# Performance work log

Measured on AMD Instinct MI355X. Metric: run time of the kernel, lower is better.

Reference implementation:

```python
import jax, jax.numpy as jnp
import numpy as np

D_MODEL = 1024
H = 16
D_K = D_MODEL // H
D_FF = 4096
EPS = 1e-6
NEG = -1.0e9


def setup_inputs() -> dict:
    key = jax.random.key(0)
    ks = jax.random.split(key, 8)
    B, S = 4, 2048
    x = jax.random.normal(ks[0], (B, S, D_MODEL), dtype=jnp.float32)
    src_mask = jnp.ones((B, 1, S, S), dtype=jnp.int32)
    s = 0.02
    wq = jax.random.normal(ks[1], (D_MODEL, D_MODEL), jnp.float32) * s
    wk = jax.random.normal(ks[2], (D_MODEL, D_MODEL), jnp.float32) * s
    wv = jax.random.normal(ks[3], (D_MODEL, D_MODEL), jnp.float32) * s
    wo = jax.random.normal(ks[4], (D_MODEL, D_MODEL), jnp.float32) * s
    w1 = jax.random.normal(ks[5], (D_MODEL, D_FF), jnp.float32) * s
    b1 = jnp.zeros((D_FF,), jnp.float32)
    w2 = jax.random.normal(ks[6], (D_FF, D_MODEL), jnp.float32) * s
    b2 = jnp.zeros((D_MODEL,), jnp.float32)
    # LayerNorm params are scalars in the original (torch.ones(1)/zeros(1))
    a1 = jnp.ones((1,), jnp.float32); bt1 = jnp.zeros((1,), jnp.float32)
    a2 = jnp.ones((1,), jnp.float32); bt2 = jnp.zeros((1,), jnp.float32)
    return {"x": x, "src_mask": src_mask, "wq": wq, "wk": wk, "wv": wv,
            "wo": wo, "w1": w1, "b1": b1, "w2": w2, "b2": b2,
            "a1": a1, "bt1": bt1, "a2": a2, "bt2": bt2}


def _layernorm(x, alpha, beta):
    # Original: (x - mean) / (std + eps), std with Bessel correction (torch default)
    mean = jnp.mean(x, axis=-1, keepdims=True)
    std = jnp.std(x, axis=-1, keepdims=True, ddof=1)
    return alpha * (x - mean) / (std + EPS) + beta


def _mha(x, mask, wq, wk, wv, wo):
    B, S, _ = x.shape
    q = (x @ wq).reshape(B, S, H, D_K).transpose(0, 2, 1, 3)  # [B,H,S,Dk]
    k = (x @ wk).reshape(B, S, H, D_K).transpose(0, 2, 1, 3)
    v = (x @ wv).reshape(B, S, H, D_K).transpose(0, 2, 1, 3)
    scores = jnp.einsum('bhqd,bhkd->bhqk', q, k) / jnp.sqrt(jnp.float32(D_K))
    scores = jnp.where(mask == 0, NEG, scores)
    attn = jax.nn.softmax(scores, axis=-1)
    out = jnp.einsum('bhqk,bhkd->bhqd', attn, v)  # [B,H,S,Dk]
    out = out.transpose(0, 2, 1, 3).reshape(B, S, D_MODEL)
    return out @ wo


def reference(x, src_mask, wq, wk, wv, wo, w1, b1, w2, b2, a1, bt1, a2, bt2):
    # Sublayer 1: self-attention with post-norm residual (dropout = eval/identity)
    attn_out = _mha(x, src_mask, wq, wk, wv, wo)
    x = _layernorm(x + attn_out, a1, bt1)
    # Sublayer 2: FFN with post-norm residual
    ffn_out = jax.nn.relu(x @ w1 + b1) @ w2 + b2
    x = _layernorm(x + ffn_out, a2, bt2)
    return x
```

## Files before the change

### kernel.cpp

```cpp
#include <hip/hip_runtime.h>
#include <stdint.h>

typedef __bf16 bf16x8 __attribute__((ext_vector_type(8)));
typedef float f32x4 __attribute__((ext_vector_type(4)));
typedef float f32x16 __attribute__((ext_vector_type(16)));
typedef unsigned short u16;
typedef u16 u16x8 __attribute__((ext_vector_type(8)));
typedef u16 u16x4 __attribute__((ext_vector_type(4)));
typedef uint32_t u32;

#define DEV __device__ __forceinline__
#define MFMA(a, b, c) __builtin_amdgcn_mfma_f32_16x16x32_bf16(a, b, c, 0, 0, 0)
#define MFMA32(a, b, c) __builtin_amdgcn_mfma_f32_32x32x16_bf16(a, b, c, 0, 0, 0)

static constexpr int B_ = 4, S_ = 2048, M_ = 8192, D_ = 1024, H_ = 16, DFF_ = 4096;

DEV u16 f2bf(float f) {
    union { float f; u32 u; } c; c.f = f;
    u32 u = c.u;
    return (u16)((u + 0x7fffu + ((u >> 16) & 1u)) >> 16);
}

DEV u32 cvt_pk_bf16(float lo, float hi) {
    u32 r;
    asm("v_cvt_pk_bf16_f32 %0, %1, %2" : "=v"(r) : "v"(lo), "v"(hi));
    return r;
}

DEV float v_exp2(float x) {
    float r;
    asm("v_exp_f32 %0, %1" : "=v"(r) : "v"(x));
    return r;
}

DEV void gload16(void* lds, const void* g) {
    __builtin_amdgcn_global_load_lds(
        (const __attribute__((address_space(1))) unsigned int*)g,
        (__attribute__((address_space(3))) unsigned int*)lds, 16, 0, 0);
}


__global__ __launch_bounds__(256) void k_pack_mask(const int* __restrict__ m,
                                                   u32* __restrict__ bits, int nwords) {
    int w = blockIdx.x * 256 + threadIdx.x;
    if (w >= nwords) return;
    const int4* s = (const int4*)(m + (size_t)w * 32);
    u32 r = 0;
#pragma unroll
    for (int j = 0; j < 8; j++) {
        int4 v = s[j];
        r |= (u32)(v.x != 0) << (j * 4) | (u32)(v.y != 0) << (j * 4 + 1) |
             (u32)(v.z != 0) << (j * 4 + 2) | (u32)(v.w != 0) << (j * 4 + 3);
    }
    bits[w] = r;
}

__global__ __launch_bounds__(256) void k_cast_bf16(const float* __restrict__ s,
                                                   u16* __restrict__ d, int n4) {
    int i = blockIdx.x * 256 + threadIdx.x;
    if (i >= n4) return;
    f32x4 v = ((const f32x4*)s)[i];
    u16x4 o;
    o[0] = f2bf(v[0]); o[1] = f2bf(v[1]); o[2] = f2bf(v[2]); o[3] = f2bf(v[3]);
    ((u16x4*)d)[i] = o;
}

__global__ void k_transpose_cast(const float* __restrict__ s, u16* __restrict__ d,
                                 int K, int N) {
    __shared__ float t[32][33];
    int n0 = blockIdx.x * 32, k0 = blockIdx.y * 32;
    int tx = threadIdx.x, ty = threadIdx.y;
#pragma unroll
    for (int i = 0; i < 4; i++)
        t[ty + i * 8][tx] = s[(size_t)(k0 + ty + i * 8) * N + n0 + tx];
    __syncthreads();
#pragma unroll
    for (int i = 0; i < 4; i++)
        d[(size_t)(n0 + ty + i * 8) * K + k0 + tx] = f2bf(t[tx][ty + i * 8]);
}

template <int EPI>
__global__ __launch_bounds__(512, 4) void k_gemm8(const u16* __restrict__ A,
                                                  const u16* __restrict__ Bt,
                                                  float* __restrict__ Cf,
                                                  u16* __restrict__ Cb,
                                                  const float* __restrict__ bias,
                                                  const float* __restrict__ resid,
                                                  u16* __restrict__ Vt,
                                                  int N, int K) {
    __shared__ u16 As[2][128 * 64];
    __shared__ u16 Bs[2][128 * 64];
    const int tid = threadIdx.x, lane = tid & 63, wave = tid >> 6;
    const int lr = lane & 15, lg = lane >> 4;
    const int wm = wave >> 1, wn = wave & 1;
    const int nbx = N >> 7;
    const int chunk = gridDim.x >> 3;
    const int id = ((int)blockIdx.x & 7) * chunk + ((int)blockIdx.x >> 3);
    const size_t row0 = (size_t)(id / nbx) * 128;
    const int col0 = (id % nbx) * 128;
    const int srow = lane >> 3;
    const int sgr = (lane & 7) ^ srow;
    const int NT = K >> 6;
    f32x4 acc[2][4] = {};

    auto stage = [&](int buf, int t) {
#pragma unroll
        for (int i = 0; i < 2; i++) {
            int c = i * 8 + wave;
            gload16((char*)&As[buf][0] + c * 1024,
                    (const char*)(A + (row0 + c * 8 + srow) * K + t * 64 + sgr * 8));
        }
#pragma unroll
        for (int i = 0; i < 2; i++) {
            int c = i * 8 + wave;
            gload16((char*)&Bs[buf][0] + c * 1024,
                    (const char*)(Bt + (size_t)(col0 + c * 8 + srow) * K + t * 64 + sgr * 8));
        }
    };

    stage(0, 0);
    for (int t = 0; t < NT; ++t) {
        const int cur = t & 1;
        if (t + 1 < NT) {
            stage(cur ^ 1, t + 1);
            asm volatile("s_waitcnt vmcnt(4)" ::: "memory");
        } else {
            asm volatile("s_waitcnt vmcnt(0)" ::: "memory");
        }
        __builtin_amdgcn_s_barrier();
        asm volatile("" ::: "memory");
        bf16x8 bF[4][2];
#pragma unroll
        for (int n = 0; n < 4; n++) {
            int r = wn * 64 + n * 16 + lr;
            int rb = r * 128, sw = (r & 7) << 4;
#pragma unroll
            for (int ks = 0; ks < 2; ks++)
                bF[n][ks] = *(const bf16x8*)((char*)&Bs[cur][0] +
                                             (rb + ((ks * 64 + lg * 16) ^ sw)));
        }
#pragma unroll
        for (int m = 0; m < 2; m++) {
            int r = wm * 32 + m * 16 + lr;
            int rb = r * 128, sw = (r & 7) << 4;
            bf16x8 a0 = *(const bf16x8*)((char*)&As[cur][0] + (rb + ((lg * 16) ^ sw)));
            bf16x8 a1 = *(const bf16x8*)((char*)&As[cur][0] + (rb + ((64 + lg * 16) ^ sw)));
            __builtin_amdgcn_s_setprio(1);
#pragma unroll
            for (int n = 0; n < 4; n++) {
                acc[m][n] = MFMA(a0, bF[n][0], acc[m][n]);
                acc[m][n] = MFMA(a1, bF[n][1], acc[m][n]);
            }
            __builtin_amdgcn_s_setprio(0);
        }
        asm volatile("" ::: "memory");
        __builtin_amdgcn_s_barrier();
    }
#pragma unroll
    for (int m = 0; m < 2; m++)
#pragma unroll
        for (int n = 0; n < 4; n++) {
            const int cg = col0 + wn * 64 + n * 16 + lr;
            const int rbase = (int)row0 + wm * 32 + m * 16 + lg * 4;
            if constexpr (EPI == 0) {
                const int proj = cg >> 10, hh = (cg >> 6) & 15, dk = cg & 63;
                const int b = rbase >> 11, s = rbase & 2047;
                if (proj == 2) {
                    u16x4 ov;
#pragma unroll
                    for (int i = 0; i < 4; i++) ov[i] = f2bf(acc[m][n][i]);
                    *(u16x4*)(Vt + ((size_t)(b * 16 + hh) * 64 + dk) * 2048 + s) = ov;
                } else {
                    const float sc = (proj == 0) ? 0.1803368801111832f : 1.f;
                    size_t base = ((size_t)(proj * 64 + b * 16 + hh) * 2048 + s) * 64 + dk;
#pragma unroll
                    for (int i = 0; i < 4; i++)
                        Cb[base + (size_t)i * 64] = f2bf(acc[m][n][i] * sc);
                }
            } else {
#pragma unroll
                for (int i = 0; i < 4; i++) {
                    const int rg = rbase + i;
                    float v = acc[m][n][i];
                    if constexpr (EPI == 1) {
                        Cf[(size_t)rg * N + cg] = v + resid[(size_t)rg * N + cg];
                    } else if constexpr (EPI == 2) {
                        v += bias[cg];
                        v = v > 0.f ? v : 0.f;
                        Cb[(size_t)rg * N + cg] = f2bf(v);
                    } else {
                        Cf[(size_t)rg * N + cg] = v + bias[cg] + resid[(size_t)rg * N + cg];
                    }
                }
            }
        }
}

template <int EPI>
__global__ __launch_bounds__(512, 2) void k_gemm256(const u16* __restrict__ A,
                                                    const u16* __restrict__ Bt,
                                                    float* __restrict__ Cf,
                                                    u16* __restrict__ Cb,
                                                    const float* __restrict__ bias,
                                                    int N, int K) {
    __shared__ u16 As[2][256 * 64];
    __shared__ u16 Bs[2][256 * 64];
    const int tid = threadIdx.x, lane = tid & 63, wave = tid >> 6;
    const int lr = lane & 15, lg = lane >> 4;
    const int wm = wave >> 2, wn = wave & 3;
    const int nbx = N >> 8;
    const int chunk = gridDim.x >> 3;
    const int id = ((int)blockIdx.x & 7) * chunk + ((int)blockIdx.x >> 3);
    const size_t row0 = (size_t)(id / nbx) * 256;
    const int col0 = (id % nbx) * 256;
    const int srow = lane >> 3;
    const int sgr = (lane & 7) ^ srow;
    const int NT = K >> 6;
    f32x4 acc[8][4] = {};

    auto stage_half = [&](int isB, int buf, int t, int h) {
        const u16* g = isB ? Bt : A;
        const size_t grow0 = isB ? (size_t)col0 : row0;
        char* base = isB ? (char*)&Bs[buf][0] : (char*)&As[buf][0];
#pragma unroll
        for (int l = 0; l < 2; l++) {
            int rt = h * 128 + l * 64 + wave * 8;
            gload16(base + rt * 128,
                    (const char*)(g + (grow0 + rt + srow) * K + t * 64 + sgr * 8));
        }
    };
    auto rdA = [&](int cur, int mh, int m, int kk) -> bf16x8 {
        int r = wm * 128 + mh * 64 + m * 16 + lr;
        int gi = kk * 4 + lg;
        return *(const bf16x8*)((char*)&As[cur][0] + r * 128 + ((gi ^ (r & 7)) << 4));
    };
    auto rdB = [&](int cur, int nh, int n, int kk) -> bf16x8 {
        int r = wn * 64 + nh * 32 + n * 16 + lr;
        int gi = kk * 4 + lg;
        return *(const bf16x8*)((char*)&Bs[cur][0] + r * 128 + ((gi ^ (r & 7)) << 4));
    };

    stage_half(0, 0, 0, 0); stage_half(0, 0, 0, 1);
    stage_half(1, 0, 0, 0); stage_half(1, 0, 0, 1);
    stage_half(1, 1, 1, 0); stage_half(1, 1, 1, 1);
    asm volatile("s_waitcnt vmcnt(4)" ::: "memory");
    __builtin_amdgcn_s_barrier();

    bf16x8 aF[4][2], b0F[2][2], b1F[2][2];
    for (int t = 0; t < NT; ++t) {
        const int cur = t & 1, nxt = cur ^ 1;
#pragma unroll
        for (int m = 0; m < 4; m++) { aF[m][0] = rdA(cur, 0, m, 0); aF[m][1] = rdA(cur, 0, m, 1); }
#pragma unroll
        for (int n = 0; n < 2; n++) { b0F[n][0] = rdB(cur, 0, n, 0); b0F[n][1] = rdB(cur, 0, n, 1); }
        if (t + 1 < NT) stage_half(0, nxt, t + 1, 0);
        __builtin_amdgcn_s_barrier();
        asm volatile("s_waitcnt lgkmcnt(0)" ::: "memory");
        __builtin_amdgcn_sched_barrier(0);
        __builtin_amdgcn_s_setprio(1);
#pragma unroll
        for (int m = 0; m < 4; m++)
#pragma unroll
            for (int n = 0; n < 2; n++) {
                acc[m][n] = MFMA(aF[m][0], b0F[n][0], acc[m][n]);
                acc[m][n] = MFMA(aF[m][1], b0F[n][1], acc[m][n]);
            }
        __builtin_amdgcn_s_setprio(0);
        __builtin_amdgcn_s_barrier();
#pragma unroll
        for (int n = 0; n < 2; n++) { b1F[n][0] = rdB(cur, 1, n, 0); b1F[n][1] = rdB(cur, 1, n, 1); }
        if (t + 1 < NT) stage_half(0, nxt, t + 1, 1);
        __builtin_amdgcn_s_barrier();
        asm volatile("s_waitcnt lgkmcnt(0)" ::: "memory");
        __builtin_amdgcn_sched_barrier(0);
        __builtin_amdgcn_s_setprio(1);
#pragma unroll
        for (int m = 0; m < 4; m++)
#pragma unroll
            for (int n = 0; n < 2; n++) {
                acc[m][2 + n] = MFMA(aF[m][0], b1F[n][0], acc[m][2 + n]);
                acc[m][2 + n] = MFMA(aF[m][1], b1F[n][1], acc[m][2 + n]);
            }
        __builtin_amdgcn_s_setprio(0);
        __builtin_amdgcn_s_barrier();
#pragma unroll
        for (int m = 0; m < 4; m++) { aF[m][0] = rdA(cur, 1, m, 0); aF[m][1] = rdA(cur, 1, m, 1); }
        if (t + 2 < NT) stage_half(1, cur, t + 2, 0);
        __builtin_amdgcn_s_barrier();
        asm volatile("s_waitcnt lgkmcnt(0)" ::: "memory");
        __builtin_amdgcn_sched_barrier(0);
        __builtin_amdgcn_s_setprio(1);
#pragma unroll
        for (int m = 0; m < 4; m++)
#pragma unroll
            for (int n = 0; n < 2; n++) {
                acc[4 + m][2 + n] = MFMA(aF[m][0], b1F[n][0], acc[4 + m][2 + n]);
                acc[4 + m][2 + n] = MFMA(aF[m][1], b1F[n][1], acc[4 + m][2 + n]);
            }
        __builtin_amdgcn_s_setprio(0);
        __builtin_amdgcn_s_barrier();
        if (t + 2 < NT) stage_half(1, cur, t + 2, 1);
        if (t + 1 < NT) {
            if (t + 2 < NT) asm volatile("s_waitcnt vmcnt(4)" ::: "memory");
            else            asm volatile("s_waitcnt vmcnt(0)" ::: "memory");
        }
        __builtin_amdgcn_s_barrier();
        __builtin_amdgcn_s_setprio(1);
#pragma unroll
        for (int m = 0; m < 4; m++)
#pragma unroll
            for (int n = 0; n < 2; n++) {
                acc[4 + m][n] = MFMA(aF[m][0], b0F[n][0], acc[4 + m][n]);
                acc[4 + m][n] = MFMA(aF[m][1], b0F[n][1], acc[4 + m][n]);
            }
        __builtin_amdgcn_s_setprio(0);
        __builtin_amdgcn_s_barrier();
    }
#pragma unroll
    for (int m = 0; m < 8; m++)
#pragma unroll
        for (int n = 0; n < 4; n++)
#pragma unroll
            for (int i = 0; i < 4; i++) {
                int rg = (int)row0 + wm * 128 + m * 16 + lg * 4 + i;
                int cg = col0 + wn * 64 + n * 16 + lr;
                float v = acc[m][n][i];
                if constexpr (EPI == 2) {
                    v += bias[cg];
                    v = v > 0.f ? v : 0.f;
                    Cb[(size_t)rg * N + cg] = f2bf(v);
                } else {
                    Cf[(size_t)rg * N + cg] = v;
                }
            }
}

__global__ __launch_bounds__(256) void k_attn(const u16* __restrict__ qkv,
                                              const u16* __restrict__ vT,
                                              const u32* __restrict__ mbits,
                                              u16* __restrict__ outb) {
    __shared__ u16 Kt[2][64 * 64];
    __shared__ u16 Vt[2][64 * 64];
    __shared__ u32 pm[2][128][2];
    const int tid = threadIdx.x, lane = tid & 63, wave = tid >> 6;
    const int l31 = lane & 31, hi = lane >> 5;
    const int id0 = blockIdx.y * 16 + blockIdx.x;
    const int id = (id0 & 7) * 128 + (id0 >> 3);
    const int bh = id >> 4;
    const int b = bh >> 4, h = bh & 15;
    const int qb0 = (id & 15) * 128;
    const size_t qbase = (size_t)bh * (2048 * 64);
    const size_t kbase = (size_t)(64 + bh) * (2048 * 64);
    const size_t vtbase = (size_t)bh * (64 * 2048);

    bf16x8 qf[4];
    const int q0 = qb0 + wave * 32;
#pragma unroll
    for (int dstep = 0; dstep < 4; dstep++)
        qf[dstep] = *(const bf16x8*)(qkv + qbase + (size_t)(q0 + l31) * 64 +
                                     dstep * 16 + hi * 8);

    u16x8 ones_u;
#pragma unroll
    for (int e = 0; e < 8; e++) ones_u[e] = 0x3f80;
    const bf16x8 ones8 = *(const bf16x8*)&ones_u;

    f32x16 o0 = {}, o1 = {}, lacc = {};
    f32x16 zin;
#pragma unroll
    for (int r = 0; r < 16; r++) zin[r] = -16.f;

    const int str = tid >> 2, sq = tid & 3;
    const int swzs = (str & 7) << 4;

    u16x8 krA, krB, vrA, vrB; u32 mwA;
    auto issue_loads = [&](int kv0n) {
        const u16* ksrc = qkv + kbase + (size_t)(kv0n + str) * 64 + sq * 16;
        krA = *(const u16x8*)ksrc; krB = *(const u16x8*)(ksrc + 8);
        const u16* vsrc = vT + vtbase + (size_t)str * 2048 + kv0n + sq * 16;
        vrA = *(const u16x8*)vsrc; vrB = *(const u16x8*)(vsrc + 8);
        mwA = mbits[(size_t)(b * 2048 + qb0 + (tid >> 1)) * 64 + (kv0n >> 5) + (tid & 1)];
    };
    auto write_tile = [&](int buf) -> bool {
        int b0 = str * 128 + sq * 32;
        *(u16x8*)((char*)&Kt[buf][0] + ((b0) ^ swzs)) = krA;
        *(u16x8*)((char*)&Kt[buf][0] + ((b0 + 16) ^ swzs)) = krB;
        *(u16x8*)((char*)&Vt[buf][0] + ((b0) ^ swzs)) = vrA;
        *(u16x8*)((char*)&Vt[buf][0] + ((b0 + 16) ^ swzs)) = vrB;
        pm[buf][tid >> 1][tid & 1] = mwA;
        return (__ballot(mwA == 0xffffffffu) == ~0ull);
    };

    const int rK0 = l31, rK1 = 32 + l31;
    const int swK0 = (rK0 & 7) << 4, swK1 = (rK1 & 7) << 4;

    issue_loads(0);
    bool aon_nxt = write_tile(0);
    for (int t = 0; t < 32; ++t) {
        const int cur = t & 1;
        const bool aon_cur = aon_nxt;
        if (t + 1 < 32) issue_loads((t + 1) * 64);
        asm volatile("s_waitcnt lgkmcnt(0)" ::: "memory");
        __builtin_amdgcn_s_barrier();

        f32x16 st0 = zin, st1 = zin;
        __builtin_amdgcn_s_setprio(1);
#pragma unroll
        for (int dstep = 0; dstep < 4; dstep++) {
            bf16x8 kf0 = *(const bf16x8*)((char*)&Kt[cur][0] + rK0 * 128 +
                                          ((dstep * 32 + hi * 16) ^ swK0));
            bf16x8 kf1 = *(const bf16x8*)((char*)&Kt[cur][0] + rK1 * 128 +
                                          ((dstep * 32 + hi * 16) ^ swK1));
            st0 = MFMA32(kf0, qf[dstep], st0);
            st1 = MFMA32(kf1, qf[dstep], st1);
        }
        __builtin_amdgcn_s_setprio(0);

        if (!aon_cur) {
            u32 mw0 = pm[cur][wave * 32 + l31][0] >> (hi * 4);
            u32 mw1 = pm[cur][wave * 32 + l31][1] >> (hi * 4);
#pragma unroll
            for (int r = 0; r < 16; r++) {
                int sh = (r & 3) + 8 * (r >> 2);
                if (!((mw0 >> sh) & 1u)) st0[r] = -1e9f;
                if (!((mw1 >> sh) & 1u)) st1[r] = -1e9f;
            }
        }
        bf16x8 pa[4];
#pragma unroll
        for (int r = 0; r < 16; r++) { st0[r] = v_exp2(st0[r]); st1[r] = v_exp2(st1[r]); }
#pragma unroll
        for (int kvb = 0; kvb < 2; kvb++) {
            const f32x16& st = kvb ? st1 : st0;
            u32 wA[4], wB[4];
#pragma unroll
            for (int g = 0; g < 4; g++) {
                wA[g] = cvt_pk_bf16(st[4 * g], st[4 * g + 1]);
                wB[g] = cvt_pk_bf16(st[4 * g + 2], st[4 * g + 3]);
            }
#pragma unroll
            for (int s = 0; s < 2; s++) {
                u32 xA = wA[2 * s], yA = wA[2 * s + 1];
                asm("v_permlane32_swap_b32 %0, %1" : "+v"(xA), "+v"(yA));
                u32 xB = wB[2 * s], yB = wB[2 * s + 1];
                asm("v_permlane32_swap_b32 %0, %1" : "+v"(xB), "+v"(yB));
                union { u32 w[4]; bf16x8 v; } pk;
                pk.w[0] = xA; pk.w[1] = xB; pk.w[2] = yA; pk.w[3] = yB;
                pa[kvb * 2 + s] = pk.v;
            }
        }
        __builtin_amdgcn_s_setprio(1);
#pragma unroll
        for (int ks = 0; ks < 4; ks++) {
            bf16x8 vb0 = *(const bf16x8*)((char*)&Vt[cur][0] + rK0 * 128 +
                                          ((ks * 32 + hi * 16) ^ swK0));
            bf16x8 vb1 = *(const bf16x8*)((char*)&Vt[cur][0] + rK1 * 128 +
                                          ((ks * 32 + hi * 16) ^ swK1));
            lacc = MFMA32(pa[ks], ones8, lacc);
            o0 = MFMA32(pa[ks], vb0, o0);
            o1 = MFMA32(pa[ks], vb1, o1);
        }
        __builtin_amdgcn_s_setprio(0);
        if (t + 1 < 32) aon_nxt = write_tile(cur ^ 1);
    }
#pragma unroll
    for (int r = 0; r < 16; r++) {
        float inv = 1.f / lacc[r];
        int qg = qb0 + wave * 32 + (r & 3) + 8 * (r >> 2) + 4 * hi;
        size_t rowb = (size_t)(b * 2048 + qg) * 1024 + h * 64 + l31;
        outb[rowb] = f2bf(o0[r] * inv);
        outb[rowb + 32] = f2bf(o1[r] * inv);
    }
}

template <bool WB>
__global__ __launch_bounds__(256) void k_ln(const float* __restrict__ tin,
                                            float* __restrict__ outf,
                                            u16* __restrict__ outb,
                                            const float* __restrict__ alpha,
                                            const float* __restrict__ beta) {
    const int row = blockIdx.x, tid = threadIdx.x;
    const f32x4 t = ((const f32x4*)(tin + (size_t)row * 1024))[tid];
    float s = t[0] + t[1] + t[2] + t[3];
    float ss = t[0] * t[0] + t[1] * t[1] + t[2] * t[2] + t[3] * t[3];
#pragma unroll
    for (int m2 = 1; m2 < 64; m2 <<= 1) {
        s += __shfl_xor(s, m2);
        ss += __shfl_xor(ss, m2);
    }
    __shared__ float ps[4], pss[4];
    if ((tid & 63) == 0) { ps[tid >> 6] = s; pss[tid >> 6] = ss; }
    __syncthreads();
    s = ps[0] + ps[1] + ps[2] + ps[3];
    ss = pss[0] + pss[1] + pss[2] + pss[3];
    const float mean = s * (1.f / 1024.f);
    float var = (ss - 1024.f * mean * mean) * (1.f / 1023.f);
    var = fmaxf(var, 0.f);
    const float inv = alpha[0] / (sqrtf(var) + 1e-6f);
    const float bet = beta[0];
    f32x4 oo;
#pragma unroll
    for (int i = 0; i < 4; i++) oo[i] = (t[i] - mean) * inv + bet;
    ((f32x4*)(outf + (size_t)row * 1024))[tid] = oo;
    if constexpr (WB) {
        u16x4 ob;
#pragma unroll
        for (int i = 0; i < 4; i++) ob[i] = f2bf(oo[i]);
        ((u16x4*)(outb + (size_t)row * 1024))[tid] = ob;
    }
}

extern "C" void kernel_launch(void* const* d_in, const int* in_sizes, int n_in,
                              void* d_out, int out_size, void* d_ws, size_t ws_size,
                              hipStream_t stream) {
    const float* x   = (const float*)d_in[0];
    const int*   msk = (const int*)d_in[1];
    const float* wq  = (const float*)d_in[2];
    const float* wk  = (const float*)d_in[3];
    const float* wv  = (const float*)d_in[4];
    const float* wo  = (const float*)d_in[5];
    const float* w1  = (const float*)d_in[6];
    const float* b1  = (const float*)d_in[7];
    const float* w2  = (const float*)d_in[8];
    const float* b2  = (const float*)d_in[9];
    const float* a1  = (const float*)d_in[10];
    const float* bt1 = (const float*)d_in[11];
    const float* a2  = (const float*)d_in[12];
    const float* bt2 = (const float*)d_in[13];
    float* out = (float*)d_out;

    char* ws = (char*)d_ws;
    size_t off = 0;
    auto alloc = [&](size_t bytes) {
        void* p = ws + off;
        off += (bytes + 255) & ~(size_t)255;
        return p;
    };
    u16* xb    = (u16*)alloc((size_t)M_ * D_ * 2);
    u16* wqkvT = (u16*)alloc((size_t)3 * D_ * D_ * 2);
    u16* woT   = (u16*)alloc((size_t)D_ * D_ * 2);
    u16* w1T   = (u16*)alloc((size_t)DFF_ * D_ * 2);
    u16* w2T   = (u16*)alloc((size_t)D_ * DFF_ * 2);
    u32* mbits = (u32*)alloc((size_t)B_ * S_ * 64 * 4);
    u16* aout  = (u16*)alloc((size_t)M_ * D_ * 2);
    float* y   = (float*)alloc((size_t)M_ * D_ * 4);
    float* x1  = (float*)alloc((size_t)M_ * D_ * 4);
    u16* x1b   = (u16*)alloc((size_t)M_ * D_ * 2);
    u16* vTb   = (u16*)alloc((size_t)64 * 64 * 2048 * 2);
    u16* qkv   = (u16*)alloc((size_t)M_ * DFF_ * 2);
    u16* hft   = qkv;

    k_pack_mask<<<dim3((B_ * S_ * 64) / 256), 256, 0, stream>>>(msk, mbits, B_ * S_ * 64);
    k_cast_bf16<<<dim3((M_ * D_ / 4) / 256), 256, 0, stream>>>(x, xb, M_ * D_ / 4);
    dim3 tb(32, 8);
    k_transpose_cast<<<dim3(32, 32), tb, 0, stream>>>(wq, wqkvT, D_, D_);
    k_transpose_cast<<<dim3(32, 32), tb, 0, stream>>>(wk, wqkvT + D_ * D_, D_, D_);
    k_transpose_cast<<<dim3(32, 32), tb, 0, stream>>>(wv, wqkvT + 2 * D_ * D_, D_, D_);
    k_transpose_cast<<<dim3(32, 32), tb, 0, stream>>>(wo, woT, D_, D_);
    k_transpose_cast<<<dim3(128, 32), tb, 0, stream>>>(w1, w1T, D_, DFF_);
    k_transpose_cast<<<dim3(32, 128), tb, 0, stream>>>(w2, w2T, DFF_, D_);

    k_gemm8<0><<<dim3(1536), 512, 0, stream>>>(xb, wqkvT, nullptr, qkv, nullptr,
                                               nullptr, vTb, 3 * D_, D_);
    k_attn<<<dim3(16, 64), 256, 0, stream>>>(qkv, vTb, mbits, aout);
    k_gemm8<1><<<dim3(512), 512, 0, stream>>>(aout, woT, y, nullptr, nullptr, x,
                                              nullptr, D_, D_);
    k_ln<true><<<dim3(M_), 256, 0, stream>>>(y, x1, x1b, a1, bt1);
    k_gemm256<2><<<dim3(512), 512, 0, stream>>>(x1b, w1T, nullptr, hft, b1, DFF_, D_);
    k_gemm8<3><<<dim3(512), 512, 0, stream>>>(hft, w2T, y, nullptr, b2, x1,
                                              nullptr, D_, DFF_);
    k_ln<false><<<dim3(M_), 256, 0, stream>>>(y, out, nullptr, a2, bt2);
}
```

Measured before the change: 412.4 us.

## Use split-K 256-tile GEMM for FFN down-projection and fuse partial sums into LayerNorm

The second FFN GEMM (K=4096) moves from the 128-tile kernel to the 256x256 tile kernel with a two-way split over K. Each half writes its own fp32 partial output, and a new LayerNorm kernel adds the two partials, the residual and the bias before normalising. The four square weight transpose-casts are also merged into one launch using a z grid dimension. The larger tiles raise data reuse, but the grid is only 256 blocks, and the extra partial buffer costs additional write and read traffic.

```diff
diff --git a/kernel.cpp b/kernel.cpp
--- a/kernel.cpp
+++ b/kernel.cpp
@@ -77,6 +77,26 @@
 #pragma unroll
     for (int i = 0; i < 4; i++)
         d[(size_t)(n0 + ty + i * 8) * K + k0 + tx] = f2bf(t[tx][ty + i * 8]);
+}
+
+__global__ void k_transpose_cast4(const float* __restrict__ s0,
+                                  const float* __restrict__ s1,
+                                  const float* __restrict__ s2,
+                                  const float* __restrict__ s3,
+                                  u16* __restrict__ dbase) {
+    __shared__ float t[32][33];
+    const int z = blockIdx.z;
+    const float* s = (z == 0) ? s0 : (z == 1) ? s1 : (z == 2) ? s2 : s3;
+    u16* d = dbase + (size_t)z * D_ * D_;
+    int n0 = blockIdx.x * 32, k0 = blockIdx.y * 32;
+    int tx = threadIdx.x, ty = threadIdx.y;
+#pragma unroll
+    for (int i = 0; i < 4; i++)
+        t[ty + i * 8][tx] = s[(size_t)(k0 + ty + i * 8) * D_ + n0 + tx];
+    __syncthreads();
+#pragma unroll
+    for (int i = 0; i < 4; i++)
+        d[(size_t)(n0 + ty + i * 8) * D_ + k0 + tx] = f2bf(t[tx][ty + i * 8]);
 }
 
 template <int EPI>
@@ -196,13 +216,14 @@
         }
 }
 
-template <int EPI>
+template <int EPI, int KSPLITS>
 __global__ __launch_bounds__(512, 2) void k_gemm256(const u16* __restrict__ A,
                                                     const u16* __restrict__ Bt,
                                                     float* __restrict__ Cf,
+                                                    float* __restrict__ Cf2,
                                                     u16* __restrict__ Cb,
                                                     const float* __restrict__ bias,
-                                                    int N, int K) {
+                                                    int N, int Keff, int lda) {
     __shared__ u16 As[2][256 * 64];
     __shared__ u16 Bs[2][256 * 64];
     const int tid = threadIdx.x, lane = tid & 63, wave = tid >> 6;
@@ -211,11 +232,14 @@
     const int nbx = N >> 8;
     const int chunk = gridDim.x >> 3;
     const int id = ((int)blockIdx.x & 7) * chunk + ((int)blockIdx.x >> 3);
-    const size_t row0 = (size_t)(id / nbx) * 256;
-    const int col0 = (id % nbx) * 256;
+    int tileid = id, ksplit = 0;
+    if constexpr (KSPLITS == 2) { ksplit = id & 1; tileid = id >> 1; }
+    const int kof = ksplit * Keff;
+    const size_t row0 = (size_t)(tileid / nbx) * 256;
+    const int col0 = (tileid % nbx) * 256;
     const int srow = lane >> 3;
     const int sgr = (lane & 7) ^ srow;
-    const int NT = K >> 6;
+    const int NT = Keff >> 6;
     f32x4 acc[8][4] = {};
 
     auto stage_half = [&](int isB, int buf, int t, int h) {
@@ -226,7 +250,7 @@
         for (int l = 0; l < 2; l++) {
             int rt = h * 128 + l * 64 + wave * 8;
             gload16(base + rt * 128,
-                    (const char*)(g + (grow0 + rt + srow) * K + t * 64 + sgr * 8));
+                    (const char*)(g + (grow0 + rt + srow) * lda + kof + t * 64 + sgr * 8));
         }
     };
     auto rdA = [&](int cur, int mh, int m, int kk) -> bf16x8 {
@@ -316,6 +340,7 @@
         __builtin_amdgcn_s_setprio(0);
         __builtin_amdgcn_s_barrier();
     }
+    float* Cout = (KSPLITS == 2 && ksplit) ? Cf2 : Cf;
 #pragma unroll
     for (int m = 0; m < 8; m++)
 #pragma unroll
@@ -330,7 +355,7 @@
                     v = v > 0.f ? v : 0.f;
                     Cb[(size_t)rg * N + cg] = f2bf(v);
                 } else {
-                    Cf[(size_t)rg * N + cg] = v;
+                    Cout[(size_t)rg * N + cg] = v;
                 }
             }
 }
@@ -508,6 +533,44 @@
         for (int i = 0; i < 4; i++) ob[i] = f2bf(oo[i]);
         ((u16x4*)(outb + (size_t)row * 1024))[tid] = ob;
     }
+}
+
+__global__ __launch_bounds__(256) void k_ln_sum2(const float* __restrict__ p0,
+                                                 const float* __restrict__ p1,
+                                                 const float* __restrict__ resid,
+                                                 const float* __restrict__ bias,
+                                                 float* __restrict__ outf,
+                                                 const float* __restrict__ alpha,
+                                                 const float* __restrict__ beta) {
+    const int row = blockIdx.x, tid = threadIdx.x;
+    const f32x4 a = ((const f32x4*)(p0 + (size_t)row * 1024))[tid];
+    const f32x4 c = ((const f32x4*)(p1 + (size_t)row * 1024))[tid];
+    const f32x4 r = ((const f32x4*)(resid + (size_t)row * 1024))[tid];
+    const f32x4 bb = ((const f32x4*)bias)[tid];
+    f32x4 t;
+#pragma unroll
+    for (int i = 0; i < 4; i++) t[i] = a[i] + c[i] + r[i] + bb[i];
+    float s = t[0] + t[1] + t[2] + t[3];
+    float ss = t[0] * t[0] + t[1] * t[1] + t[2] * t[2] + t[3] * t[3];
+#pragma unroll
+    for (int m2 = 1; m2 < 64; m2 <<= 1) {
+        s += __shfl_xor(s, m2);
+        ss += __shfl_xor(ss, m2);
+    }
+    __shared__ float ps[4], pss[4];
+    if ((tid & 63) == 0) { ps[tid >> 6] = s; pss[tid >> 6] = ss; }
+    __syncthreads();
+    s = ps[0] + ps[1] + ps[2] + ps[3];
+    ss = pss[0] + pss[1] + pss[2] + pss[3];
+    const float mean = s * (1.f / 1024.f);
+    float var = (ss - 1024.f * mean * mean) * (1.f / 1023.f);
+    var = fmaxf(var, 0.f);
+    const float inv = alpha[0] / (sqrtf(var) + 1e-6f);
+    const float bet = beta[0];
+    f32x4 oo;
+#pragma unroll
+    for (int i = 0; i < 4; i++) oo[i] = (t[i] - mean) * inv + bet;
+    ((f32x4*)(outf + (size_t)row * 1024))[tid] = oo;
 }
 
 extern "C" void kernel_launch(void* const* d_in, const int* in_sizes, int n_in,
@@ -544,6 +607,7 @@
     u32* mbits = (u32*)alloc((size_t)B_ * S_ * 64 * 4);
     u16* aout  = (u16*)alloc((size_t)M_ * D_ * 2);
     float* y   = (float*)alloc((size_t)M_ * D_ * 4);
+    float* y1  = (float*)alloc((size_t)M_ * D_ * 4);
     float* x1  = (float*)alloc((size_t)M_ * D_ * 4);
     u16* x1b   = (u16*)alloc((size_t)M_ * D_ * 2);
     u16* vTb   = (u16*)alloc((size_t)64 * 64 * 2048 * 2);
@@ -553,10 +617,7 @@
     k_pack_mask<<<dim3((B_ * S_ * 64) / 256), 256, 0, stream>>>(msk, mbits, B_ * S_ * 64);
     k_cast_bf16<<<dim3((M_ * D_ / 4) / 256), 256, 0, stream>>>(x, xb, M_ * D_ / 4);
     dim3 tb(32, 8);
-    k_transpose_cast<<<dim3(32, 32), tb, 0, stream>>>(wq, wqkvT, D_, D_);
-    k_transpose_cast<<<dim3(32, 32), tb, 0, stream>>>(wk, wqkvT + D_ * D_, D_, D_);
-    k_transpose_cast<<<dim3(32, 32), tb, 0, stream>>>(wv, wqkvT + 2 * D_ * D_, D_, D_);
-    k_transpose_cast<<<dim3(32, 32), tb, 0, stream>>>(wo, woT, D_, D_);
+    k_transpose_cast4<<<dim3(32, 32, 4), tb, 0, stream>>>(wq, wk, wv, wo, wqkvT);
     k_transpose_cast<<<dim3(128, 32), tb, 0, stream>>>(w1, w1T, D_, DFF_);
     k_transpose_cast<<<dim3(32, 128), tb, 0, stream>>>(w2, w2T, DFF_, D_);
 
@@ -566,8 +627,9 @@
     k_gemm8<1><<<dim3(512), 512, 0, stream>>>(aout, woT, y, nullptr, nullptr, x,
                                               nullptr, D_, D_);
     k_ln<true><<<dim3(M_), 256, 0, stream>>>(y, x1, x1b, a1, bt1);
-    k_gemm256<2><<<dim3(512), 512, 0, stream>>>(x1b, w1T, nullptr, hft, b1, DFF_, D_);
-    k_gemm8<3><<<dim3(512), 512, 0, stream>>>(hft, w2T, y, nullptr, b2, x1,
-                                              nullptr, D_, DFF_);
-    k_ln<false><<<dim3(M_), 256, 0, stream>>>(y, out, nullptr, a2, bt2);
-}
+    k_gemm256<2, 1><<<dim3(512), 512, 0, stream>>>(x1b, w1T, nullptr, nullptr, hft,
+                                                   b1, DFF_, D_, D_);
+    k_gemm256<3, 2><<<dim3(256), 512, 0, stream>>>(hft, w2T, y, y1, nullptr,
+                                                   nullptr, D_, DFF_ / 2, DFF_);
+    k_ln_sum2<<<dim3(M_), 256, 0, stream>>>(y, y1, x1, b2, out, a2, bt2);
+}
```

Result: no change. 412.2 us (-0.1%).
